# Optimization experiments

Hardware: AMD Instinct MI355X
Metric: run time of the kernel (lower is better)

The kernel has to match this reference:

```python
import jax, jax.numpy as jnp
import numpy as np

N_NODES = 100000

def spmm(edge_row, edge_col, edge_val, dense):
    # sparse [N,N] @ dense [N,D] via gather + segment_sum
    msgs = edge_val[:, None] * dense[edge_col]          # [E, D]
    return jax.ops.segment_sum(msgs, edge_row, num_segments=N_NODES)

def setup_inputs() -> dict:
    key = jax.random.key(0)
    ks = jax.random.split(key, 6)
    N, F, H, C, E = N_NODES, 512, 256, 40, 3200000
    x = jax.random.normal(ks[0], (N, F), dtype=jnp.float32)
    edge_row = jax.random.randint(ks[1], (E,), 0, N, dtype=jnp.int32)
    edge_col = jax.random.randint(ks[2], (E,), 0, N, dtype=jnp.int32)
    edge_val = jax.random.uniform(ks[3], (E,), dtype=jnp.float32)
    # xavier_uniform init for conv weights, zeros for biases
    lim1 = float(np.sqrt(6.0 / (F + H)))
    lim2 = float(np.sqrt(6.0 / (H + C)))
    W1 = jax.random.uniform(ks[4], (F, H), minval=-lim1, maxval=lim1, dtype=jnp.float32)
    b1 = jnp.zeros((H,), dtype=jnp.float32)
    W2 = jax.random.uniform(ks[5], (H, C), minval=-lim2, maxval=lim2, dtype=jnp.float32)
    b2 = jnp.zeros((C,), dtype=jnp.float32)
    return {"x": x, "edge_row": edge_row, "edge_col": edge_col, "edge_val": edge_val,
            "W1": W1, "b1": b1, "W2": W2, "b2": b2}

def reference(x, edge_row, edge_col, edge_val, W1, b1, W2, b2):
    # layer 1: dense transform, sparse aggregation, bias, relu (dropout = identity in eval)
    h = spmm(edge_row, edge_col, edge_val, x @ W1) + b1   # [N, H]
    h = jax.nn.relu(h)
    mid = h
    # layer 2
    out = spmm(edge_row, edge_col, edge_val, h @ W2) + b2  # [N, C]
    return (mid, out)  # out.squeeze(1) is a no-op for C>1
```

## Files before the change

kernel.cpp:

```cpp
#include <hip/hip_runtime.h>


typedef __bf16 bf16;
typedef __bf16 bf16x8 __attribute__((ext_vector_type(8)));
typedef float floatx4 __attribute__((ext_vector_type(4)));
typedef float floatx2 __attribute__((ext_vector_type(2)));

#define NBMAX 400

__global__ __launch_bounds__(256) void conv_w(const float* __restrict__ W1,
                                              const float* __restrict__ W2,
                                              bf16* __restrict__ W1T,
                                              bf16* __restrict__ W2T) {
  int i = blockIdx.x * 256 + threadIdx.x;
  if (i < 512 * 256) {
    int k = i >> 8, n = i & 255;
    W1T[n * 512 + k] = (bf16)W1[i];
  }
  int j = i - 512 * 256;
  if (j >= 0 && j < 48 * 256) {
    int n = j >> 8, k = j & 255;
    W2T[j] = (n < 40) ? (bf16)W2[k * 40 + n] : (bf16)0.0f;
  }
}

__global__ __launch_bounds__(256) void bhist_kernel(const int* __restrict__ er,
                                                    int* __restrict__ gbcount,
                                                    int* __restrict__ blkcnt,
                                                    int E, int NB, int EBLK) {
  __shared__ int cnt[NBMAX];
  const int t = threadIdx.x;
  for (int b = t; b < NB; b += 256) cnt[b] = 0;
  __syncthreads();
  const int base = blockIdx.x * 8192;
#pragma unroll
  for (int k = 0; k < 8; k++) {
    int i = base + k * 1024 + t * 4;
    if (i < E) {
      int4 r = *(const int4*)(er + i);
      atomicAdd(&cnt[r.x >> 8], 1);
      atomicAdd(&cnt[r.y >> 8], 1);
      atomicAdd(&cnt[r.z >> 8], 1);
      atomicAdd(&cnt[r.w >> 8], 1);
    }
  }
  __syncthreads();
  for (int b = t; b < NB; b += 256) {
    int c = cnt[b];
    blkcnt[b * EBLK + blockIdx.x] = c;
    if (c) atomicAdd(&gbcount[b], c);
  }
}

__global__ __launch_bounds__(512) void bscan_kernel(const int* __restrict__ gbcount,
                                                    int* __restrict__ bstart, int NB) {
  __shared__ int wsum[8];
  const int t = threadIdx.x;
  const int lane = t & 63, wave = t >> 6;
  int v = (t < NB) ? gbcount[t] : 0;
  int incl = v;
#pragma unroll
  for (int d = 1; d < 64; d <<= 1) {
    int o = __shfl_up(incl, d, 64);
    if (lane >= d) incl += o;
  }
  if (lane == 63) wsum[wave] = incl;
  __syncthreads();
  int off = 0;
#pragma unroll
  for (int w = 0; w < 8; w++)
    if (w < wave) off += wsum[w];
  int excl = off + incl - v;
  if (t <= NB) bstart[t] = excl;
}

__global__ __launch_bounds__(512) void bscan2_kernel(const int* __restrict__ blkcnt,
                                                     const int* __restrict__ bstart,
                                                     int* __restrict__ blkoff, int EBLK) {
  __shared__ int wsum[8];
  const int b = blockIdx.x, t = threadIdx.x;
  const int lane = t & 63, wave = t >> 6;
  int v = (t < EBLK) ? blkcnt[b * EBLK + t] : 0;
  int incl = v;
#pragma unroll
  for (int d = 1; d < 64; d <<= 1) {
    int o = __shfl_up(incl, d, 64);
    if (lane >= d) incl += o;
  }
  if (lane == 63) wsum[wave] = incl;
  __syncthreads();
  int off = 0;
#pragma unroll
  for (int w = 0; w < 8; w++)
    if (w < wave) off += wsum[w];
  if (t < EBLK) blkoff[b * EBLK + t] = bstart[b] + off + incl - v;
}

__global__ __launch_bounds__(256) void partA_kernel(
    const int* __restrict__ er, const int* __restrict__ ec, const float* __restrict__ ev,
    const int* __restrict__ blkoff, int2* __restrict__ epack_b, int E, int NB, int EBLK) {
  __shared__ int cur[NBMAX];
  const int t = threadIdx.x;
  for (int b = t; b < NB; b += 256) cur[b] = blkoff[b * EBLK + blockIdx.x];
  __syncthreads();
  const int base = blockIdx.x * 8192;
#pragma unroll
  for (int k = 0; k < 8; k++) {
    int i = base + k * 1024 + t * 4;
    if (i < E) {
      int4 r = *(const int4*)(er + i);
      int4 c = *(const int4*)(ec + i);
      float4 v = *(const float4*)(ev + i);
      int s0 = atomicAdd(&cur[r.x >> 8], 1);
      epack_b[s0] = make_int2(((r.x & 255) << 17) | c.x, __float_as_int(v.x));
      int s1 = atomicAdd(&cur[r.y >> 8], 1);
      epack_b[s1] = make_int2(((r.y & 255) << 17) | c.y, __float_as_int(v.y));
      int s2 = atomicAdd(&cur[r.z >> 8], 1);
      epack_b[s2] = make_int2(((r.z & 255) << 17) | c.z, __float_as_int(v.z));
      int s3 = atomicAdd(&cur[r.w >> 8], 1);
      epack_b[s3] = make_int2(((r.w & 255) << 17) | c.w, __float_as_int(v.w));
    }
  }
}

__global__ __launch_bounds__(256) void partB_kernel(
    const int2* __restrict__ epack_b, const int* __restrict__ bstart,
    int2* __restrict__ epack_f, int* __restrict__ rp, int M) {
  __shared__ int rcnt[256];
  __shared__ int rcur[256];
  __shared__ int wsum[4];
  const int b = blockIdx.x, t = threadIdx.x;
  const int s = bstart[b];
  const int e_ = bstart[b + 1];
  rcnt[t] = 0;
  __syncthreads();
  for (int i = s + t; i < e_; i += 256) {
    unsigned int ro = ((unsigned int)epack_b[i].x) >> 17;
    atomicAdd(&rcnt[ro], 1);
  }
  __syncthreads();
  const int lane = t & 63, wave = t >> 6;
  int v = rcnt[t];
  int incl = v;
#pragma unroll
  for (int d = 1; d < 64; d <<= 1) {
    int o = __shfl_up(incl, d, 64);
    if (lane >= d) incl += o;
  }
  if (lane == 63) wsum[wave] = incl;
  __syncthreads();
  int off = 0;
#pragma unroll
  for (int w = 0; w < 4; w++)
    if (w < wave) off += wsum[w];
  rcur[t] = s + off + incl - v;
  __syncthreads();
  for (int i = s + t; i < e_; i += 256) {
    int2 m = epack_b[i];
    unsigned int ro = ((unsigned int)m.x) >> 17;
    int slot = atomicAdd(&rcur[ro], 1);
    epack_f[slot] = make_int2(m.x & 0x1FFFF, m.y);
  }
  __syncthreads();
  int r = (b << 8) + t;
  if (r < M) rp[r] = rcur[t];
}

__global__ __launch_bounds__(256) void gemm1_kernel(const float* __restrict__ x,
                                                    const bf16* __restrict__ W1T,
                                                    unsigned int* __restrict__ T1f8, int M) {
  __shared__ __align__(16) bf16 As[64][40];
  __shared__ __align__(16) bf16 Bs[256][40];
  const int t = threadIdx.x;
  const int wave = t >> 6, lane = t & 63;
  const int quad = lane >> 4, l16 = lane & 15;
  const int m0 = blockIdx.x * 64;
  floatx4 acc[16] = {};

  const int ar = t >> 2, aq = t & 3;
  const int a_gr = m0 + ar;
  const float* a_src = x + (size_t)a_gr * 512 + aq * 8;
  const bf16* b_src = W1T + (size_t)t * 512;

  for (int k0 = 0; k0 < 512; k0 += 32) {
    __syncthreads();
    {
      float4 f0 = {0,0,0,0}, f1 = {0,0,0,0};
      if (a_gr < M) {
        const float4* p = (const float4*)(a_src + k0);
        f0 = p[0]; f1 = p[1];
      }
      bf16x8 av;
      av[0] = (bf16)f0.x; av[1] = (bf16)f0.y; av[2] = (bf16)f0.z; av[3] = (bf16)f0.w;
      av[4] = (bf16)f1.x; av[5] = (bf16)f1.y; av[6] = (bf16)f1.z; av[7] = (bf16)f1.w;
      *(bf16x8*)&As[ar][aq * 8] = av;
    }
    {
      const bf16* p = b_src + k0;
      bf16x8 q0 = *(const bf16x8*)(p);
      bf16x8 q1 = *(const bf16x8*)(p + 8);
      bf16x8 q2 = *(const bf16x8*)(p + 16);
      bf16x8 q3 = *(const bf16x8*)(p + 24);
      *(bf16x8*)&Bs[t][0]  = q0;
      *(bf16x8*)&Bs[t][8]  = q1;
      *(bf16x8*)&Bs[t][16] = q2;
      *(bf16x8*)&Bs[t][24] = q3;
    }
    __syncthreads();
    bf16x8 a = *(const bf16x8*)&As[wave * 16 + l16][quad * 8];
#pragma unroll
    for (int nt = 0; nt < 16; nt++) {
      bf16x8 b = *(const bf16x8*)&Bs[nt * 16 + l16][quad * 8];
      acc[nt] = __builtin_amdgcn_mfma_f32_16x16x32_bf16(a, b, acc[nt], 0, 0, 0);
    }
  }
  const int row_base = m0 + wave * 16 + quad * 4;
#pragma unroll
  for (int nt0 = 0; nt0 < 4; nt0++) {
#pragma unroll
    for (int j = 0; j < 4; j++) {
      int gr = row_base + j;
      if (gr < M) {
        int p = 0;
        p = __builtin_amdgcn_cvt_pk_fp8_f32(acc[nt0][j],     acc[nt0 + 4][j],  p, false);
        p = __builtin_amdgcn_cvt_pk_fp8_f32(acc[nt0 + 8][j], acc[nt0 + 12][j], p, true);
        T1f8[(size_t)gr * 64 + nt0 * 16 + l16] = (unsigned int)p;
      }
    }
  }
}

__global__ __launch_bounds__(256, 6) void spmm1_kernel(
    const int* __restrict__ rp, const int2* __restrict__ epack,
    const unsigned int* __restrict__ T1f8, const float* __restrict__ b1,
    float* __restrict__ mid, int M) {
  const int lane = threadIdx.x & 63;
  const int r = blockIdx.x * 4 + (threadIdx.x >> 6);
  if (r >= M) return;
  const int eend = rp[r];
  int e = (r == 0) ? 0 : rp[r - 1];
  float a0 = 0.f, a1 = 0.f, a2 = 0.f, a3 = 0.f;
  if (e < eend && (e & 1)) {
    int2 m = epack[e];
    float v = __int_as_float(m.y);
    unsigned int u = T1f8[(((unsigned)m.x) << 6) | lane];
    floatx2 lo = __builtin_amdgcn_cvt_pk_f32_fp8(u, false);
    floatx2 hi = __builtin_amdgcn_cvt_pk_f32_fp8(u, true);
    a0 += v * lo[0]; a1 += v * lo[1]; a2 += v * hi[0]; a3 += v * hi[1];
    e++;
  }
  for (; e + 15 < eend; e += 16) {
    int4 pA = *(const int4*)(epack + e);
    int4 pB = *(const int4*)(epack + e + 2);
    int4 pC = *(const int4*)(epack + e + 4);
    int4 pD = *(const int4*)(epack + e + 6);
    int4 pE = *(const int4*)(epack + e + 8);
    int4 pF = *(const int4*)(epack + e + 10);
    int4 pG = *(const int4*)(epack + e + 12);
    int4 pH = *(const int4*)(epack + e + 14);
    unsigned int u0  = T1f8[(((unsigned)pA.x) << 6) | lane];
    unsigned int u1  = T1f8[(((unsigned)pA.z) << 6) | lane];
    unsigned int u2  = T1f8[(((unsigned)pB.x) << 6) | lane];
    unsigned int u3  = T1f8[(((unsigned)pB.z) << 6) | lane];
    unsigned int u4  = T1f8[(((unsigned)pC.x) << 6) | lane];
    unsigned int u5  = T1f8[(((unsigned)pC.z) << 6) | lane];
    unsigned int u6  = T1f8[(((unsigned)pD.x) << 6) | lane];
    unsigned int u7  = T1f8[(((unsigned)pD.z) << 6) | lane];
    unsigned int u8  = T1f8[(((unsigned)pE.x) << 6) | lane];
    unsigned int u9  = T1f8[(((unsigned)pE.z) << 6) | lane];
    unsigned int u10 = T1f8[(((unsigned)pF.x) << 6) | lane];
    unsigned int u11 = T1f8[(((unsigned)pF.z) << 6) | lane];
    unsigned int u12 = T1f8[(((unsigned)pG.x) << 6) | lane];
    unsigned int u13 = T1f8[(((unsigned)pG.z) << 6) | lane];
    unsigned int u14 = T1f8[(((unsigned)pH.x) << 6) | lane];
    unsigned int u15 = T1f8[(((unsigned)pH.z) << 6) | lane];
    float v0  = __int_as_float(pA.y), v1  = __int_as_float(pA.w);
    float v2  = __int_as_float(pB.y), v3  = __int_as_float(pB.w);
    float v4  = __int_as_float(pC.y), v5  = __int_as_float(pC.w);
    float v6  = __int_as_float(pD.y), v7  = __int_as_float(pD.w);
    float v8  = __int_as_float(pE.y), v9  = __int_as_float(pE.w);
    float v10 = __int_as_float(pF.y), v11 = __int_as_float(pF.w);
    float v12 = __int_as_float(pG.y), v13 = __int_as_float(pG.w);
    float v14 = __int_as_float(pH.y), v15 = __int_as_float(pH.w);
    floatx2 lo, hi;
    lo = __builtin_amdgcn_cvt_pk_f32_fp8(u0, false);
    hi = __builtin_amdgcn_cvt_pk_f32_fp8(u0, true);
    a0 += v0 * lo[0]; a1 += v0 * lo[1]; a2 += v0 * hi[0]; a3 += v0 * hi[1];
    lo = __builtin_amdgcn_cvt_pk_f32_fp8(u1, false);
    hi = __builtin_amdgcn_cvt_pk_f32_fp8(u1, true);
    a0 += v1 * lo[0]; a1 += v1 * lo[1]; a2 += v1 * hi[0]; a3 += v1 * hi[1];
    lo = __builtin_amdgcn_cvt_pk_f32_fp8(u2, false);
    hi = __builtin_amdgcn_cvt_pk_f32_fp8(u2, true);
    a0 += v2 * lo[0]; a1 += v2 * lo[1]; a2 += v2 * hi[0]; a3 += v2 * hi[1];
    lo = __builtin_amdgcn_cvt_pk_f32_fp8(u3, false);
    hi = __builtin_amdgcn_cvt_pk_f32_fp8(u3, true);
    a0 += v3 * lo[0]; a1 += v3 * lo[1]; a2 += v3 * hi[0]; a3 += v3 * hi[1];
    lo = __builtin_amdgcn_cvt_pk_f32_fp8(u4, false);
    hi = __builtin_amdgcn_cvt_pk_f32_fp8(u4, true);
    a0 += v4 * lo[0]; a1 += v4 * lo[1]; a2 += v4 * hi[0]; a3 += v4 * hi[1];
    lo = __builtin_amdgcn_cvt_pk_f32_fp8(u5, false);
    hi = __builtin_amdgcn_cvt_pk_f32_fp8(u5, true);
    a0 += v5 * lo[0]; a1 += v5 * lo[1]; a2 += v5 * hi[0]; a3 += v5 * hi[1];
    lo = __builtin_amdgcn_cvt_pk_f32_fp8(u6, false);
    hi = __builtin_amdgcn_cvt_pk_f32_fp8(u6, true);
    a0 += v6 * lo[0]; a1 += v6 * lo[1]; a2 += v6 * hi[0]; a3 += v6 * hi[1];
    lo = __builtin_amdgcn_cvt_pk_f32_fp8(u7, false);
    hi = __builtin_amdgcn_cvt_pk_f32_fp8(u7, true);
    a0 += v7 * lo[0]; a1 += v7 * lo[1]; a2 += v7 * hi[0]; a3 += v7 * hi[1];
    lo = __builtin_amdgcn_cvt_pk_f32_fp8(u8, false);
    hi = __builtin_amdgcn_cvt_pk_f32_fp8(u8, true);
    a0 += v8 * lo[0]; a1 += v8 * lo[1]; a2 += v8 * hi[0]; a3 += v8 * hi[1];
    lo = __builtin_amdgcn_cvt_pk_f32_fp8(u9, false);
    hi = __builtin_amdgcn_cvt_pk_f32_fp8(u9, true);
    a0 += v9 * lo[0]; a1 += v9 * lo[1]; a2 += v9 * hi[0]; a3 += v9 * hi[1];
    lo = __builtin_amdgcn_cvt_pk_f32_fp8(u10, false);
    hi = __builtin_amdgcn_cvt_pk_f32_fp8(u10, true);
    a0 += v10 * lo[0]; a1 += v10 * lo[1]; a2 += v10 * hi[0]; a3 += v10 * hi[1];
    lo = __builtin_amdgcn_cvt_pk_f32_fp8(u11, false);
    hi = __builtin_amdgcn_cvt_pk_f32_fp8(u11, true);
    a0 += v11 * lo[0]; a1 += v11 * lo[1]; a2 += v11 * hi[0]; a3 += v11 * hi[1];
    lo = __builtin_amdgcn_cvt_pk_f32_fp8(u12, false);
    hi = __builtin_amdgcn_cvt_pk_f32_fp8(u12, true);
    a0 += v12 * lo[0]; a1 += v12 * lo[1]; a2 += v12 * hi[0]; a3 += v12 * hi[1];
    lo = __builtin_amdgcn_cvt_pk_f32_fp8(u13, false);
    hi = __builtin_amdgcn_cvt_pk_f32_fp8(u13, true);
    a0 += v13 * lo[0]; a1 += v13 * lo[1]; a2 += v13 * hi[0]; a3 += v13 * hi[1];
    lo = __builtin_amdgcn_cvt_pk_f32_fp8(u14, false);
    hi = __builtin_amdgcn_cvt_pk_f32_fp8(u14, true);
    a0 += v14 * lo[0]; a1 += v14 * lo[1]; a2 += v14 * hi[0]; a3 += v14 * hi[1];
    lo = __builtin_amdgcn_cvt_pk_f32_fp8(u15, false);
    hi = __builtin_amdgcn_cvt_pk_f32_fp8(u15, true);
    a0 += v15 * lo[0]; a1 += v15 * lo[1]; a2 += v15 * hi[0]; a3 += v15 * hi[1];
  }
  for (; e + 7 < eend; e += 8) {
    int4 p01 = *(const int4*)(epack + e);
    int4 p23 = *(const int4*)(epack + e + 2);
    int4 p45 = *(const int4*)(epack + e + 4);
    int4 p67 = *(const int4*)(epack + e + 6);
    unsigned int u0 = T1f8[(((unsigned)p01.x) << 6) | lane];
    unsigned int u1 = T1f8[(((unsigned)p01.z) << 6) | lane];
    unsigned int u2 = T1f8[(((unsigned)p23.x) << 6) | lane];
    unsigned int u3 = T1f8[(((unsigned)p23.z) << 6) | lane];
    unsigned int u4 = T1f8[(((unsigned)p45.x) << 6) | lane];
    unsigned int u5 = T1f8[(((unsigned)p45.z) << 6) | lane];
    unsigned int u6 = T1f8[(((unsigned)p67.x) << 6) | lane];
    unsigned int u7 = T1f8[(((unsigned)p67.z) << 6) | lane];
    float v0 = __int_as_float(p01.y), v1 = __int_as_float(p01.w);
    float v2 = __int_as_float(p23.y), v3 = __int_as_float(p23.w);
    float v4 = __int_as_float(p45.y), v5 = __int_as_float(p45.w);
    float v6 = __int_as_float(p67.y), v7 = __int_as_float(p67.w);
    floatx2 lo, hi;
    lo = __builtin_amdgcn_cvt_pk_f32_fp8(u0, false);
    hi = __builtin_amdgcn_cvt_pk_f32_fp8(u0, true);
    a0 += v0 * lo[0]; a1 += v0 * lo[1]; a2 += v0 * hi[0]; a3 += v0 * hi[1];
    lo = __builtin_amdgcn_cvt_pk_f32_fp8(u1, false);
    hi = __builtin_amdgcn_cvt_pk_f32_fp8(u1, true);
    a0 += v1 * lo[0]; a1 += v1 * lo[1]; a2 += v1 * hi[0]; a3 += v1 * hi[1];
    lo = __builtin_amdgcn_cvt_pk_f32_fp8(u2, false);
    hi = __builtin_amdgcn_cvt_pk_f32_fp8(u2, true);
    a0 += v2 * lo[0]; a1 += v2 * lo[1]; a2 += v2 * hi[0]; a3 += v2 * hi[1];
    lo = __builtin_amdgcn_cvt_pk_f32_fp8(u3, false);
    hi = __builtin_amdgcn_cvt_pk_f32_fp8(u3, true);
    a0 += v3 * lo[0]; a1 += v3 * lo[1]; a2 += v3 * hi[0]; a3 += v3 * hi[1];
    lo = __builtin_amdgcn_cvt_pk_f32_fp8(u4, false);
    hi = __builtin_amdgcn_cvt_pk_f32_fp8(u4, true);
    a0 += v4 * lo[0]; a1 += v4 * lo[1]; a2 += v4 * hi[0]; a3 += v4 * hi[1];
    lo = __builtin_amdgcn_cvt_pk_f32_fp8(u5, false);
    hi = __builtin_amdgcn_cvt_pk_f32_fp8(u5, true);
    a0 += v5 * lo[0]; a1 += v5 * lo[1]; a2 += v5 * hi[0]; a3 += v5 * hi[1];
    lo = __builtin_amdgcn_cvt_pk_f32_fp8(u6, false);
    hi = __builtin_amdgcn_cvt_pk_f32_fp8(u6, true);
    a0 += v6 * lo[0]; a1 += v6 * lo[1]; a2 += v6 * hi[0]; a3 += v6 * hi[1];
    lo = __builtin_amdgcn_cvt_pk_f32_fp8(u7, false);
    hi = __builtin_amdgcn_cvt_pk_f32_fp8(u7, true);
    a0 += v7 * lo[0]; a1 += v7 * lo[1]; a2 += v7 * hi[0]; a3 += v7 * hi[1];
  }
  for (; e + 3 < eend; e += 4) {
    int4 p01 = *(const int4*)(epack + e);
    int4 p23 = *(const int4*)(epack + e + 2);
    unsigned int u0 = T1f8[(((unsigned)p01.x) << 6) | lane];
    unsigned int u1 = T1f8[(((unsigned)p01.z) << 6) | lane];
    unsigned int u2 = T1f8[(((unsigned)p23.x) << 6) | lane];
    unsigned int u3 = T1f8[(((unsigned)p23.z) << 6) | lane];
    float v0 = __int_as_float(p01.y), v1 = __int_as_float(p01.w);
    float v2 = __int_as_float(p23.y), v3 = __int_as_float(p23.w);
    floatx2 lo, hi;
    lo = __builtin_amdgcn_cvt_pk_f32_fp8(u0, false);
    hi = __builtin_amdgcn_cvt_pk_f32_fp8(u0, true);
    a0 += v0 * lo[0]; a1 += v0 * lo[1]; a2 += v0 * hi[0]; a3 += v0 * hi[1];
    lo = __builtin_amdgcn_cvt_pk_f32_fp8(u1, false);
    hi = __builtin_amdgcn_cvt_pk_f32_fp8(u1, true);
    a0 += v1 * lo[0]; a1 += v1 * lo[1]; a2 += v1 * hi[0]; a3 += v1 * hi[1];
    lo = __builtin_amdgcn_cvt_pk_f32_fp8(u2, false);
    hi = __builtin_amdgcn_cvt_pk_f32_fp8(u2, true);
    a0 += v2 * lo[0]; a1 += v2 * lo[1]; a2 += v2 * hi[0]; a3 += v2 * hi[1];
    lo = __builtin_amdgcn_cvt_pk_f32_fp8(u3, false);
    hi = __builtin_amdgcn_cvt_pk_f32_fp8(u3, true);
    a0 += v3 * lo[0]; a1 += v3 * lo[1]; a2 += v3 * hi[0]; a3 += v3 * hi[1];
  }
  for (; e < eend; e++) {
    int2 m = epack[e];
    float v = __int_as_float(m.y);
    unsigned int u = T1f8[(((unsigned)m.x) << 6) | lane];
    floatx2 lo = __builtin_amdgcn_cvt_pk_f32_fp8(u, false);
    floatx2 hi = __builtin_amdgcn_cvt_pk_f32_fp8(u, true);
    a0 += v * lo[0]; a1 += v * lo[1]; a2 += v * hi[0]; a3 += v * hi[1];
  }
  float o0 = fmaxf(a0 + b1[lane],       0.f);
  float o1 = fmaxf(a1 + b1[lane + 64],  0.f);
  float o2 = fmaxf(a2 + b1[lane + 128], 0.f);
  float o3 = fmaxf(a3 + b1[lane + 192], 0.f);
  float* mrow = mid + (size_t)r * 256 + lane;
  mrow[0]   = o0;
  mrow[64]  = o1;
  mrow[128] = o2;
  mrow[192] = o3;
}

__global__ __launch_bounds__(256) void gemm2_kernel(const float* __restrict__ mid,
                                                    const bf16* __restrict__ W2T,
                                                    unsigned int* __restrict__ T2f8, int M) {
  __shared__ __align__(16) bf16 As[64][40];
  __shared__ __align__(16) bf16 Bs[48][40];
  const int t = threadIdx.x;
  const int wave = t >> 6, lane = t & 63;
  const int quad = lane >> 4, l16 = lane & 15;
  const int m0 = blockIdx.x * 64;
  floatx4 acc[3] = {};
  const int ar = t >> 2, aq = t & 3;
  const int a_gr = m0 + ar;
  const float* a_src = mid + (size_t)a_gr * 256 + aq * 8;

  for (int k0 = 0; k0 < 256; k0 += 32) {
    __syncthreads();
    {
      float4 f0 = {0,0,0,0}, f1 = {0,0,0,0};
      if (a_gr < M) {
        const float4* p = (const float4*)(a_src + k0);
        f0 = p[0]; f1 = p[1];
      }
      bf16x8 av;
      av[0] = (bf16)f0.x; av[1] = (bf16)f0.y; av[2] = (bf16)f0.z; av[3] = (bf16)f0.w;
      av[4] = (bf16)f1.x; av[5] = (bf16)f1.y; av[6] = (bf16)f1.z; av[7] = (bf16)f1.w;
      *(bf16x8*)&As[ar][aq * 8] = av;
    }
    if (t < 192) {
      int n = t >> 2, q = t & 3;
      bf16x8 b = *(const bf16x8*)(W2T + n * 256 + k0 + q * 8);
      *(bf16x8*)&Bs[n][q * 8] = b;
    }
    __syncthreads();
    bf16x8 a = *(const bf16x8*)&As[wave * 16 + l16][quad * 8];
#pragma unroll
    for (int nt = 0; nt < 3; nt++) {
      bf16x8 b = *(const bf16x8*)&Bs[nt * 16 + l16][quad * 8];
      acc[nt] = __builtin_amdgcn_mfma_f32_16x16x32_bf16(a, b, acc[nt], 0, 0, 0);
    }
  }
  const int row_base = m0 + wave * 16 + quad * 4;
#pragma unroll
  for (int j = 0; j < 4; j++) {
    int gr = row_base + j;
    if (gr < M) {
      int p = 0;
      p = __builtin_amdgcn_cvt_pk_fp8_f32(acc[0][j], acc[1][j], p, false);
      p = __builtin_amdgcn_cvt_pk_fp8_f32(acc[2][j], 0.0f,      p, true);
      T2f8[(size_t)gr * 16 + l16] = (unsigned int)p;
    }
  }
}

__global__ __launch_bounds__(256, 6) void spmm2_kernel(
    const int* __restrict__ rp, const int2* __restrict__ epack,
    const unsigned int* __restrict__ T2f8, const float* __restrict__ b2,
    float* __restrict__ out2, int M) {
  const int lane = threadIdx.x & 63;
  const int r = blockIdx.x * 4 + (threadIdx.x >> 6);
  if (r >= M) return;
  const int q = lane & 15;
  const int g = lane >> 4;
  const int eend = rp[r];
  int e = (r == 0) ? 0 : rp[r - 1];
  float a0 = 0.f, a1 = 0.f, a2 = 0.f;
  if (e < eend && (e & 1)) {
    if (g == 0) {
      int2 m = epack[e];
      float v = __int_as_float(m.y);
      unsigned int u = T2f8[(((unsigned)m.x) << 4) | q];
      floatx2 lo = __builtin_amdgcn_cvt_pk_f32_fp8(u, false);
      floatx2 hi = __builtin_amdgcn_cvt_pk_f32_fp8(u, true);
      a0 += v * lo[0]; a1 += v * lo[1]; a2 += v * hi[0];
    }
    e++;
  }
  for (; e + 15 < eend; e += 16) {
    int4 m0 = *(const int4*)(epack + e + 2 * g);
    int4 m1 = *(const int4*)(epack + e + 8 + 2 * g);
    unsigned int u0 = T2f8[(((unsigned)m0.x) << 4) | q];
    unsigned int u1 = T2f8[(((unsigned)m0.z) << 4) | q];
    unsigned int u2 = T2f8[(((unsigned)m1.x) << 4) | q];
    unsigned int u3 = T2f8[(((unsigned)m1.z) << 4) | q];
    float v0 = __int_as_float(m0.y), v1 = __int_as_float(m0.w);
    float v2 = __int_as_float(m1.y), v3 = __int_as_float(m1.w);
    floatx2 lo, hi;
    lo = __builtin_amdgcn_cvt_pk_f32_fp8(u0, false);
    hi = __builtin_amdgcn_cvt_pk_f32_fp8(u0, true);
    a0 += v0 * lo[0]; a1 += v0 * lo[1]; a2 += v0 * hi[0];
    lo = __builtin_amdgcn_cvt_pk_f32_fp8(u1, false);
    hi = __builtin_amdgcn_cvt_pk_f32_fp8(u1, true);
    a0 += v1 * lo[0]; a1 += v1 * lo[1]; a2 += v1 * hi[0];
    lo = __builtin_amdgcn_cvt_pk_f32_fp8(u2, false);
    hi = __builtin_amdgcn_cvt_pk_f32_fp8(u2, true);
    a0 += v2 * lo[0]; a1 += v2 * lo[1]; a2 += v2 * hi[0];
    lo = __builtin_amdgcn_cvt_pk_f32_fp8(u3, false);
    hi = __builtin_amdgcn_cvt_pk_f32_fp8(u3, true);
    a0 += v3 * lo[0]; a1 += v3 * lo[1]; a2 += v3 * hi[0];
  }
  for (; e + 7 < eend; e += 8) {
    int4 m = *(const int4*)(epack + e + 2 * g);
    float v0 = __int_as_float(m.y), v1 = __int_as_float(m.w);
    unsigned int u0 = T2f8[(((unsigned)m.x) << 4) | q];
    unsigned int u1 = T2f8[(((unsigned)m.z) << 4) | q];
    floatx2 l0 = __builtin_amdgcn_cvt_pk_f32_fp8(u0, false);
    floatx2 h0 = __builtin_amdgcn_cvt_pk_f32_fp8(u0, true);
    floatx2 l1 = __builtin_amdgcn_cvt_pk_f32_fp8(u1, false);
    floatx2 h1 = __builtin_amdgcn_cvt_pk_f32_fp8(u1, true);
    a0 += v0 * l0[0]; a1 += v0 * l0[1]; a2 += v0 * h0[0];
    a0 += v1 * l1[0]; a1 += v1 * l1[1]; a2 += v1 * h1[0];
  }
  for (; e + 3 < eend; e += 4) {
    int2 m = epack[e + g];
    float v = __int_as_float(m.y);
    unsigned int u = T2f8[(((unsigned)m.x) << 4) | q];
    floatx2 lo = __builtin_amdgcn_cvt_pk_f32_fp8(u, false);
    floatx2 hi = __builtin_amdgcn_cvt_pk_f32_fp8(u, true);
    a0 += v * lo[0]; a1 += v * lo[1]; a2 += v * hi[0];
  }
  if (e + g < eend) {
    int2 m = epack[e + g];
    float v = __int_as_float(m.y);
    unsigned int u = T2f8[(((unsigned)m.x) << 4) | q];
    floatx2 lo = __builtin_amdgcn_cvt_pk_f32_fp8(u, false);
    floatx2 hi = __builtin_amdgcn_cvt_pk_f32_fp8(u, true);
    a0 += v * lo[0]; a1 += v * lo[1]; a2 += v * hi[0];
  }
  a0 += __shfl_down(a0, 32, 64); a0 += __shfl_down(a0, 16, 64);
  a1 += __shfl_down(a1, 32, 64); a1 += __shfl_down(a1, 16, 64);
  a2 += __shfl_down(a2, 32, 64); a2 += __shfl_down(a2, 16, 64);
  if (lane < 16) {
    float* orow = out2 + (size_t)r * 40;
    orow[lane]      = a0 + b2[lane];
    orow[lane + 16] = a1 + b2[lane + 16];
    if (lane < 8) orow[lane + 32] = a2 + b2[lane + 32];
  }
}

extern "C" void kernel_launch(void* const* d_in, const int* in_sizes, int n_in,
                              void* d_out, int out_size, void* d_ws, size_t ws_size,
                              hipStream_t stream) {
  const float* x        = (const float*)d_in[0];
  const int*   edge_row = (const int*)d_in[1];
  const int*   edge_col = (const int*)d_in[2];
  const float* edge_val = (const float*)d_in[3];
  const float* W1       = (const float*)d_in[4];
  const float* b1       = (const float*)d_in[5];
  const float* W2       = (const float*)d_in[6];
  const float* b2       = (const float*)d_in[7];
  const int M = in_sizes[0] / 512;
  const int E = in_sizes[1];
  const int NB = (M + 255) >> 8;
  const int EBLK = (E + 8191) / 8192;

  char* ws = (char*)d_ws;
  size_t off = 0;
  bf16* W1T     = (bf16*)(ws + off);  off += 512 * 256 * 2;
  bf16* W2T     = (bf16*)(ws + off);  off += 48 * 256 * 2;
  unsigned int* T1f8 = (unsigned int*)(ws + off); off += (size_t)M * 256;
  unsigned int* T2f8 = (unsigned int*)(ws + off); off += (size_t)M * 64;
  int* rp       = (int*)(ws + off);   off += (size_t)M * 4;
  int* gbcount  = (int*)(ws + off);   off += NBMAX * 4;
  int* bstart   = (int*)(ws + off);   off += (NBMAX + 1) * 4;
  int* blkcnt   = (int*)(ws + off);   off += (size_t)NB * EBLK * 4;
  int* blkoff   = (int*)(ws + off);   off += (size_t)NB * EBLK * 4;
  off = (off + 15) & ~(size_t)15;
  int2* epack_b = (int2*)(ws + off);  off += (size_t)E * 8;
  int2* epack_f = (int2*)(ws + off);  off += (size_t)E * 8;

  float* mid  = (float*)d_out;
  float* out2 = mid + (size_t)M * 256;

  hipMemsetAsync(gbcount, 0, NBMAX * 4, stream);
  conv_w<<<(512 * 256 + 48 * 256 + 255) / 256, 256, 0, stream>>>(W1, W2, W1T, W2T);
  bhist_kernel<<<EBLK, 256, 0, stream>>>(edge_row, gbcount, blkcnt, E, NB, EBLK);
  bscan_kernel<<<1, 512, 0, stream>>>(gbcount, bstart, NB);
  bscan2_kernel<<<NB, 512, 0, stream>>>(blkcnt, bstart, blkoff, EBLK);
  partA_kernel<<<EBLK, 256, 0, stream>>>(edge_row, edge_col, edge_val,
                                         blkoff, epack_b, E, NB, EBLK);
  partB_kernel<<<NB, 256, 0, stream>>>(epack_b, bstart, epack_f, rp, M);
  gemm1_kernel<<<(M + 63) / 64, 256, 0, stream>>>(x, W1T, T1f8, M);
  spmm1_kernel<<<(M + 3) / 4, 256, 0, stream>>>(rp, epack_f, T1f8, b1, mid, M);
  gemm2_kernel<<<(M + 63) / 64, 256, 0, stream>>>(mid, W2T, T2f8, M);
  spmm2_kernel<<<(M + 3) / 4, 256, 0, stream>>>(rp, epack_f, T2f8, b2, out2, M);
}
```

Measured before the change: 658.0 us.

## Load GEMM operands directly into MFMA registers, removing LDS staging and barriers

Both dense GEMM kernels stop staging A and B tiles through shared memory. Each lane now loads its own A fragment from global memory, converts it to bf16, and reads B fragments straight from the transposed weight array (expected to sit in cache). This removes two __syncthreads per k-step and the LDS traffic, and launch bounds now request 4 blocks per CU. The cost is more global/L2 loads for B, since every wave fetches the full weight tile instead of sharing one copy per block.

```diff
diff --git a/kernel.cpp b/kernel.cpp
--- a/kernel.cpp
+++ b/kernel.cpp
@@ -166,51 +166,34 @@
   if (r < M) rp[r] = rcur[t];
 }
 
-__global__ __launch_bounds__(256) void gemm1_kernel(const float* __restrict__ x,
-                                                    const bf16* __restrict__ W1T,
-                                                    unsigned int* __restrict__ T1f8, int M) {
-  __shared__ __align__(16) bf16 As[64][40];
-  __shared__ __align__(16) bf16 Bs[256][40];
+__global__ __launch_bounds__(256, 4) void gemm1_kernel(const float* __restrict__ x,
+                                                       const bf16* __restrict__ W1T,
+                                                       unsigned int* __restrict__ T1f8, int M) {
   const int t = threadIdx.x;
   const int wave = t >> 6, lane = t & 63;
   const int quad = lane >> 4, l16 = lane & 15;
   const int m0 = blockIdx.x * 64;
   floatx4 acc[16] = {};
 
-  const int ar = t >> 2, aq = t & 3;
-  const int a_gr = m0 + ar;
-  const float* a_src = x + (size_t)a_gr * 512 + aq * 8;
-  const bf16* b_src = W1T + (size_t)t * 512;
+  const int arow = m0 + wave * 16 + l16;
+  const bool arow_ok = (arow < M);
+  const float* a_src = x + (size_t)arow * 512 + quad * 8;
+  const bf16* b_base = W1T + (size_t)l16 * 512 + quad * 8;
 
   for (int k0 = 0; k0 < 512; k0 += 32) {
-    __syncthreads();
+    bf16x8 a;
     {
-      float4 f0 = {0,0,0,0}, f1 = {0,0,0,0};
-      if (a_gr < M) {
+      float4 f0 = {0, 0, 0, 0}, f1 = {0, 0, 0, 0};
+      if (arow_ok) {
         const float4* p = (const float4*)(a_src + k0);
         f0 = p[0]; f1 = p[1];
       }
-      bf16x8 av;
-      av[0] = (bf16)f0.x; av[1] = (bf16)f0.y; av[2] = (bf16)f0.z; av[3] = (bf16)f0.w;
-      av[4] = (bf16)f1.x; av[5] = (bf16)f1.y; av[6] = (bf16)f1.z; av[7] = (bf16)f1.w;
-      *(bf16x8*)&As[ar][aq * 8] = av;
-    }
-    {
-      const bf16* p = b_src + k0;
-      bf16x8 q0 = *(const bf16x8*)(p);
-      bf16x8 q1 = *(const bf16x8*)(p + 8);
-      bf16x8 q2 = *(const bf16x8*)(p + 16);
-      bf16x8 q3 = *(const bf16x8*)(p + 24);
-      *(bf16x8*)&Bs[t][0]  = q0;
-      *(bf16x8*)&Bs[t][8]  = q1;
-      *(bf16x8*)&Bs[t][16] = q2;
-      *(bf16x8*)&Bs[t][24] = q3;
-    }
-    __syncthreads();
-    bf16x8 a = *(const bf16x8*)&As[wave * 16 + l16][quad * 8];
+      a[0] = (bf16)f0.x; a[1] = (bf16)f0.y; a[2] = (bf16)f0.z; a[3] = (bf16)f0.w;
+      a[4] = (bf16)f1.x; a[5] = (bf16)f1.y; a[6] = (bf16)f1.z; a[7] = (bf16)f1.w;
+    }
 #pragma unroll
     for (int nt = 0; nt < 16; nt++) {
-      bf16x8 b = *(const bf16x8*)&Bs[nt * 16 + l16][quad * 8];
+      bf16x8 b = *(const bf16x8*)(b_base + (size_t)nt * 16 * 512 + k0);
       acc[nt] = __builtin_amdgcn_mfma_f32_16x16x32_bf16(a, b, acc[nt], 0, 0, 0);
     }
   }
@@ -417,43 +400,34 @@
   mrow[192] = o3;
 }
 
-__global__ __launch_bounds__(256) void gemm2_kernel(const float* __restrict__ mid,
-                                                    const bf16* __restrict__ W2T,
-                                                    unsigned int* __restrict__ T2f8, int M) {
-  __shared__ __align__(16) bf16 As[64][40];
-  __shared__ __align__(16) bf16 Bs[48][40];
+__global__ __launch_bounds__(256, 4) void gemm2_kernel(const float* __restrict__ mid,
+                                                       const bf16* __restrict__ W2T,
+                                                       unsigned int* __restrict__ T2f8, int M) {
   const int t = threadIdx.x;
   const int wave = t >> 6, lane = t & 63;
   const int quad = lane >> 4, l16 = lane & 15;
   const int m0 = blockIdx.x * 64;
   floatx4 acc[3] = {};
-  const int ar = t >> 2, aq = t & 3;
-  const int a_gr = m0 + ar;
-  const float* a_src = mid + (size_t)a_gr * 256 + aq * 8;
+
+  const int arow = m0 + wave * 16 + l16;
+  const bool arow_ok = (arow < M);
+  const float* a_src = mid + (size_t)arow * 256 + quad * 8;
+  const bf16* b_base = W2T + (size_t)l16 * 256 + quad * 8;
 
   for (int k0 = 0; k0 < 256; k0 += 32) {
-    __syncthreads();
+    bf16x8 a;
     {
-      float4 f0 = {0,0,0,0}, f1 = {0,0,0,0};
-      if (a_gr < M) {
+      float4 f0 = {0, 0, 0, 0}, f1 = {0, 0, 0, 0};
+      if (arow_ok) {
         const float4* p = (const float4*)(a_src + k0);
         f0 = p[0]; f1 = p[1];
       }
-      bf16x8 av;
-      av[0] = (bf16)f0.x; av[1] = (bf16)f0.y; av[2] = (bf16)f0.z; av[3] = (bf16)f0.w;
-      av[4] = (bf16)f1.x; av[5] = (bf16)f1.y; av[6] = (bf16)f1.z; av[7] = (bf16)f1.w;
-      *(bf16x8*)&As[ar][aq * 8] = av;
-    }
-    if (t < 192) {
-      int n = t >> 2, q = t & 3;
-      bf16x8 b = *(const bf16x8*)(W2T + n * 256 + k0 + q * 8);
-      *(bf16x8*)&Bs[n][q * 8] = b;
-    }
-    __syncthreads();
-    bf16x8 a = *(const bf16x8*)&As[wave * 16 + l16][quad * 8];
+      a[0] = (bf16)f0.x; a[1] = (bf16)f0.y; a[2] = (bf16)f0.z; a[3] = (bf16)f0.w;
+      a[4] = (bf16)f1.x; a[5] = (bf16)f1.y; a[6] = (bf16)f1.z; a[7] = (bf16)f1.w;
+    }
 #pragma unroll
     for (int nt = 0; nt < 3; nt++) {
-      bf16x8 b = *(const bf16x8*)&Bs[nt * 16 + l16][quad * 8];
+      bf16x8 b = *(const bf16x8*)(b_base + (size_t)nt * 16 * 256 + k0);
       acc[nt] = __builtin_amdgcn_mfma_f32_16x16x32_bf16(a, b, acc[nt], 0, 0, 0);
     }
   }
```

Result: slower. 808.0 us (+22.8%).
